# Performance work log

Measured on AMD Instinct MI355X. Metric: run time of the kernel, lower is better.

## Reference

```python
import jax, jax.numpy as jnp
import numpy as np

B = 64          # number of scenes/graphs
OBJS = 2048     # objects per scene
N = B * OBJS    # total objects
D = 256         # representation_dim
K = 2           # num_channels


def setup_inputs() -> dict:
    key = jax.random.key(0)
    k1, k2, k3 = jax.random.split(key, 3)
    x_aggregation = jax.random.normal(k1, (N, D), dtype=jnp.float32)
    num_objs = jnp.full((B,), OBJS, dtype=jnp.int32)
    # glorot for att_shared [1, D]: fan_in + fan_out = 1 + D
    std_shared = float(np.sqrt(6.0 / (1 + D)))
    att_shared = jax.random.uniform(k2, (1, D), dtype=jnp.float32,
                                    minval=-std_shared, maxval=std_shared)
    # glorot for att_scale [K, 1]
    std_scale = float(np.sqrt(6.0 / (K + 1)))
    att_scale = jax.random.uniform(k3, (K, 1), dtype=jnp.float32,
                                   minval=-std_scale, maxval=std_scale)
    channel_bias = jnp.zeros((K, D), dtype=jnp.float32)
    return {"x_aggregation": x_aggregation, "num_objs": num_objs,
            "att_shared": att_shared, "att_scale": att_scale,
            "channel_bias": channel_bias}


def reference(x_aggregation, num_objs, att_shared, att_scale, channel_bias):
    batch_idx = jnp.repeat(jnp.arange(B), num_objs, total_repeat_length=N)  # [N]
    # scatter_mean: per-scene context features [B, D]
    seg_sum = jax.ops.segment_sum(x_aggregation, batch_idx, num_segments=B)
    counts = jnp.maximum(num_objs, 1).astype(x_aggregation.dtype)
    ctx = seg_sum / counts[:, None]
    attn_in = jax.nn.leaky_relu(x_aggregation + ctx[batch_idx], negative_slope=0.2)  # [N, D]
    # per-channel logits: ((attn_in + bias[k]) . att_shared) * scale[k]
    base = attn_in @ att_shared[0]                 # [N]
    bias_term = channel_bias @ att_shared[0]       # [K]
    logits = (base[:, None] + bias_term[None, :]) * att_scale[:, 0][None, :]  # [N, K]
    # per-channel segment softmax over objects within each scene
    m = jax.ops.segment_max(logits, batch_idx, num_segments=B)   # [B, K]
    z = jnp.exp(logits - m[batch_idx])
    s = jax.ops.segment_sum(z, batch_idx, num_segments=B)        # [B, K]
    attn_weights = z / s[batch_idx]                              # [N, K]
    # attention-weighted pooling per channel -> [B, D, K]
    weighted = x_aggregation[:, :, None] * attn_weights[:, None, :]  # [N, D, K]
    scene_features = jax.ops.segment_sum(weighted, batch_idx, num_segments=B)
    return scene_features, attn_weights
```

## Files before the change

kernel.cpp:

```cpp
#include <hip/hip_runtime.h>

#define B    64
#define OBJS 2048
#define NTOT (B * OBJS)
#define D    256
#define K    2
#define S1   16
#define CH   (OBJS / S1)
#define RPW  (CH / 4)

#define WS_P1  0
#define WS_UP  (1024 * 256)
#define WS_ZP  (WS_UP + 1024 * 512)
#define WS_E   (WS_ZP + 1024 * 8)

static __device__ __forceinline__ float lrelu02(float v) {
    return v > 0.0f ? v : 0.2f * v;
}

__global__ __launch_bounds__(256) void k1_partial(const float* __restrict__ x,
                                                  float* __restrict__ ws) {
    __shared__ float red[4 * D];
    int blk = blockIdx.x;
    int w = threadIdx.x >> 6, l = threadIdx.x & 63;
    int row0 = blk * CH + w * RPW;

    float4 acc = make_float4(0.f, 0.f, 0.f, 0.f);
    const float* px = x + (size_t)row0 * D + 4 * l;
#pragma unroll 8
    for (int j = 0; j < RPW; ++j) {
        float4 v = *(const float4*)(px + (size_t)j * D);
        acc.x += v.x; acc.y += v.y; acc.z += v.z; acc.w += v.w;
    }
    *(float4*)(red + w * D + 4 * l) = acc;
    __syncthreads();
    int t = threadIdx.x;
    if (t < 64) {
        float4 a = ((const float4*)(red        ))[t];
        float4 e = ((const float4*)(red +     D))[t];
        float4 f = ((const float4*)(red + 2 * D))[t];
        float4 g = ((const float4*)(red + 3 * D))[t];
        float4 s = make_float4(a.x + e.x + f.x + g.x, a.y + e.y + f.y + g.y,
                               a.z + e.z + f.z + g.z, a.w + e.w + f.w + g.w);
        *(float4*)(ws + WS_P1 + blk * D + 4 * t) = s;
    }
}

__global__ __launch_bounds__(256) void k2_main(const float* __restrict__ x,
                                               const int* __restrict__ num_objs,
                                               const float* __restrict__ att_scale,
                                               const float* __restrict__ att_shared,
                                               const float* __restrict__ channel_bias,
                                               float* __restrict__ ws) {
    __shared__ float pl[4 * 576];
    __shared__ float esm[4 * 16];
    __shared__ float sctx[D];
    __shared__ float sbt[2];

    int blk = blockIdx.x;
    int b = blk >> 4;
    int t = threadIdx.x;
    int w = t >> 6, l = t & 63;
    int r = l & 7, s = l >> 3;
    int row0 = blk * CH + w * RPW;

    {
        int cnt = num_objs[b]; if (cnt < 1) cnt = 1;
        float inv = 1.0f / (float)cnt;
        float sum = 0.f;
#pragma unroll
        for (int c = 0; c < S1; ++c) sum += ws[WS_P1 + (b * S1 + c) * D + t];
        sctx[t] = sum * inv;
    }
    if (t < 64) {
        float4 a = ((const float4*)att_shared)[t];
#pragma unroll
        for (int k = 0; k < K; ++k) {
            float4 cb = ((const float4*)(channel_bias + k * D))[t];
            float v = a.x * cb.x + a.y * cb.y + a.z * cb.z + a.w * cb.w;
#pragma unroll
            for (int m = 32; m > 0; m >>= 1) v += __shfl_xor(v, m);
            if (t == 0) sbt[k] = v;
        }
    }
    __syncthreads();

    float4 a4   = ((const float4*)att_shared)[l];
    float4 ctx4 = *(const float4*)(sctx + 4 * l);
    float bt0 = sbt[0], bt1 = sbt[1];
    float s0 = att_scale[0], s1 = att_scale[1];

    float4 acc0 = make_float4(0.f, 0.f, 0.f, 0.f);
    float4 acc1 = make_float4(0.f, 0.f, 0.f, 0.f);
    float z0 = 0.f, z1 = 0.f;
    float e0c = 0.f, e1c = 0.f;
    float* pw = pl  + w * 576;
    float* ew = esm + w * 16;
    const float* px = x + (size_t)row0 * D + 4 * l;

#pragma unroll
    for (int g = 0; g < 4; ++g) {
        float4 v0 = *(const float4*)(px + (size_t)(g * 8 + 0) * D);
        float4 v1 = *(const float4*)(px + (size_t)(g * 8 + 1) * D);
        float4 v2 = *(const float4*)(px + (size_t)(g * 8 + 2) * D);
        float4 v3 = *(const float4*)(px + (size_t)(g * 8 + 3) * D);
        float4 v4 = *(const float4*)(px + (size_t)(g * 8 + 4) * D);
        float4 v5 = *(const float4*)(px + (size_t)(g * 8 + 5) * D);
        float4 v6 = *(const float4*)(px + (size_t)(g * 8 + 6) * D);
        float4 v7 = *(const float4*)(px + (size_t)(g * 8 + 7) * D);

#define PDOT(V) (lrelu02((V).x + ctx4.x) * a4.x + lrelu02((V).y + ctx4.y) * a4.y \
               + lrelu02((V).z + ctx4.z) * a4.z + lrelu02((V).w + ctx4.w) * a4.w)
        pw[l * 9 + 0] = PDOT(v0); pw[l * 9 + 1] = PDOT(v1);
        pw[l * 9 + 2] = PDOT(v2); pw[l * 9 + 3] = PDOT(v3);
        pw[l * 9 + 4] = PDOT(v4); pw[l * 9 + 5] = PDOT(v5);
        pw[l * 9 + 6] = PDOT(v6); pw[l * 9 + 7] = PDOT(v7);
#undef PDOT
        float tr = 0.f;
#pragma unroll
        for (int q = 0; q < 8; ++q) tr += pw[(s * 8 + q) * 9 + r];
        tr += __shfl_xor(tr, 8);
        tr += __shfl_xor(tr, 16);
        tr += __shfl_xor(tr, 32);

        float e0 = __expf((tr + bt0) * s0);
        float e1 = __expf((tr + bt1) * s1);
        if (((l >> 3) & 3) == g) { e0c = e0; e1c = e1; }
        if (l < 8) { ew[2 * l] = e0; ew[2 * l + 1] = e1; }
        float4 E0 = *(const float4*)(ew + 0);
        float4 E1 = *(const float4*)(ew + 4);
        float4 E2 = *(const float4*)(ew + 8);
        float4 E3 = *(const float4*)(ew + 12);
        z0 += E0.x + E0.z + E1.x + E1.z + E2.x + E2.z + E3.x + E3.z;
        z1 += E0.y + E0.w + E1.y + E1.w + E2.y + E2.w + E3.y + E3.w;

#define ACC(V, EA, EB) { acc0.x += (V).x * (EA); acc0.y += (V).y * (EA);      \
                         acc0.z += (V).z * (EA); acc0.w += (V).w * (EA);      \
                         acc1.x += (V).x * (EB); acc1.y += (V).y * (EB);      \
                         acc1.z += (V).z * (EB); acc1.w += (V).w * (EB); }
        ACC(v0, E0.x, E0.y) ACC(v1, E0.z, E0.w)
        ACC(v2, E1.x, E1.y) ACC(v3, E1.z, E1.w)
        ACC(v4, E2.x, E2.y) ACC(v5, E2.z, E2.w)
        ACC(v6, E3.x, E3.y) ACC(v7, E3.z, E3.w)
#undef ACC
    }

    if (l < 32) ((float2*)(ws + WS_E))[row0 + l] = make_float2(e0c, e1c);
    if (l == 0) {
        ws[WS_ZP + blk * 8 + w * 2 + 0] = z0;
        ws[WS_ZP + blk * 8 + w * 2 + 1] = z1;
    }
    __syncthreads();
    {
        int base = w * (D * K) + l * 8;
        pl[base + 0] = acc0.x; pl[base + 1] = acc1.x;
        pl[base + 2] = acc0.y; pl[base + 3] = acc1.y;
        pl[base + 4] = acc0.z; pl[base + 5] = acc1.z;
        pl[base + 6] = acc0.w; pl[base + 7] = acc1.w;
    }
    __syncthreads();
    if (t < 128) {
        float4 a = ((const float4*)(pl       ))[t];
        float4 e = ((const float4*)(pl +  512))[t];
        float4 f = ((const float4*)(pl + 1024))[t];
        float4 g = ((const float4*)(pl + 1536))[t];
        float4 s4 = make_float4(a.x + e.x + f.x + g.x, a.y + e.y + f.y + g.y,
                                a.z + e.z + f.z + g.z, a.w + e.w + f.w + g.w);
        *(float4*)(ws + WS_UP + (size_t)blk * (D * K) + 4 * t) = s4;
    }
}

__global__ __launch_bounds__(256) void k3_final(const float* __restrict__ ws,
                                                float* __restrict__ out) {
    __shared__ float zsh[2];
    int b = blockIdx.x;
    int t = threadIdx.x;
    int w = t >> 6, l = t & 63;

    if (w < 2) {
        float v = ws[WS_ZP + (b * S1 + (l >> 2)) * 8 + (l & 3) * 2 + w];
#pragma unroll
        for (int m = 32; m > 0; m >>= 1) v += __shfl_xor(v, m);
        if (l == 0) zsh[w] = v;
    }
    __syncthreads();
    float z0 = zsh[0], z1 = zsh[1];
    float iz0 = 1.0f / z0, iz1 = 1.0f / z1;

#pragma unroll
    for (int j = t; j < D * K; j += 256) {
        float s = 0.f;
#pragma unroll
        for (int c = 0; c < S1; ++c) s += ws[WS_UP + (b * S1 + c) * (D * K) + j];
        out[b * (D * K) + j] = s * ((j & 1) ? iz1 : iz0);
    }
    const float4* E = (const float4*)(ws + WS_E);
    float4* W = (float4*)(out + B * D * K);
#pragma unroll
    for (int i = t; i < OBJS / 2; i += 256) {
        float4 e = E[b * (OBJS / 2) + i];
        W[b * (OBJS / 2) + i] = make_float4(e.x * iz0, e.y * iz1, e.z * iz0, e.w * iz1);
    }
}

extern "C" void kernel_launch(void* const* d_in, const int* in_sizes, int n_in,
                              void* d_out, int out_size, void* d_ws, size_t ws_size,
                              hipStream_t stream) {
    const float* x            = (const float*)d_in[0];
    const int*   num_objs     = (const int*)d_in[1];
    const float* att_shared   = (const float*)d_in[2];
    const float* att_scale    = (const float*)d_in[3];
    const float* channel_bias = (const float*)d_in[4];
    float* ws  = (float*)d_ws;
    float* out = (float*)d_out;

    k1_partial<<<B * S1, 256, 0, stream>>>(x, ws);
    k2_main<<<B * S1, 256, 0, stream>>>(x, num_objs, att_scale, att_shared,
                                        channel_bias, ws);
    k3_final<<<B, 256, 0, stream>>>(ws, out);
}
```

Before: 221.4 us.

## Fuse three kernels into one cooperative kernel with per-scene atomic barriers

Merges the partial-sum, main attention, and final normalization kernels into a single cooperative launch. Blocks of one scene sync on an atomic counter spin-wait before computing context, and the last block of each scene to finish (found with a second atomic counter) does the final reduction and write-out. This removes two kernel launch boundaries and their tail idle time. In exchange it adds a memset, spin-wait costs, and a dependence on all 1024 blocks being co-resident.

```diff
diff --git a/kernel.cpp b/kernel.cpp
--- a/kernel.cpp
+++ b/kernel.cpp
@@ -13,9 +13,205 @@
 #define WS_UP  (1024 * 256)
 #define WS_ZP  (WS_UP + 1024 * 512)
 #define WS_E   (WS_ZP + 1024 * 8)
+#define WS_CNT (WS_E + NTOT * 2)
 
 static __device__ __forceinline__ float lrelu02(float v) {
     return v > 0.0f ? v : 0.2f * v;
+}
+
+__global__ __launch_bounds__(256, 4) void fused_all(
+        const float* __restrict__ x,
+        const int* __restrict__ num_objs,
+        const float* __restrict__ att_scale,
+        const float* __restrict__ att_shared,
+        const float* __restrict__ channel_bias,
+        float* __restrict__ ws,
+        float* __restrict__ out) {
+    __shared__ float pl[4 * 576];
+    __shared__ float esm[4 * 16];
+    __shared__ float sctx[D];
+    __shared__ float sbt[2];
+    __shared__ int   sfin;
+
+    int blk = blockIdx.x;
+    int b = blk >> 4;
+    int t = threadIdx.x;
+    int w = t >> 6, l = t & 63;
+    int r = l & 7, sl = l >> 3;
+    int row0 = blk * CH + w * RPW;
+    int* cntA = (int*)(ws + WS_CNT);
+    int* cntF = cntA + B;
+
+    {
+        float4 acc = make_float4(0.f, 0.f, 0.f, 0.f);
+        const float* px = x + (size_t)row0 * D + 4 * l;
+#pragma unroll 8
+        for (int j = 0; j < RPW; ++j) {
+            float4 v = *(const float4*)(px + (size_t)j * D);
+            acc.x += v.x; acc.y += v.y; acc.z += v.z; acc.w += v.w;
+        }
+        *(float4*)(pl + w * D + 4 * l) = acc;
+        __syncthreads();
+        if (t < 64) {
+            float4 a = ((const float4*)(pl        ))[t];
+            float4 e = ((const float4*)(pl +     D))[t];
+            float4 f = ((const float4*)(pl + 2 * D))[t];
+            float4 g = ((const float4*)(pl + 3 * D))[t];
+            float4 s4 = make_float4(a.x + e.x + f.x + g.x, a.y + e.y + f.y + g.y,
+                                    a.z + e.z + f.z + g.z, a.w + e.w + f.w + g.w);
+            *(float4*)(ws + WS_P1 + blk * D + 4 * t) = s4;
+        }
+        __syncthreads();
+        if (t == 0) {
+            __threadfence();
+            atomicAdd(&cntA[b], 1);
+            while (__hip_atomic_load(&cntA[b], __ATOMIC_RELAXED,
+                                     __HIP_MEMORY_SCOPE_AGENT) < S1)
+                __builtin_amdgcn_s_sleep(2);
+            __threadfence();
+        }
+        __syncthreads();
+    }
+
+    {
+        int cnt = num_objs[b]; if (cnt < 1) cnt = 1;
+        float inv = 1.0f / (float)cnt;
+        float sum = 0.f;
+#pragma unroll
+        for (int c = 0; c < S1; ++c) sum += ws[WS_P1 + (b * S1 + c) * D + t];
+        sctx[t] = sum * inv;
+    }
+    if (t < 64) {
+        float4 a = ((const float4*)att_shared)[t];
+#pragma unroll
+        for (int k = 0; k < K; ++k) {
+            float4 cb = ((const float4*)(channel_bias + k * D))[t];
+            float v = a.x * cb.x + a.y * cb.y + a.z * cb.z + a.w * cb.w;
+#pragma unroll
+            for (int m = 32; m > 0; m >>= 1) v += __shfl_xor(v, m);
+            if (t == 0) sbt[k] = v;
+        }
+    }
+    __syncthreads();
+
+    float4 a4   = ((const float4*)att_shared)[l];
+    float4 ctx4 = *(const float4*)(sctx + 4 * l);
+    float bt0 = sbt[0], bt1 = sbt[1];
+    float s0 = att_scale[0], s1 = att_scale[1];
+
+    float4 acc0 = make_float4(0.f, 0.f, 0.f, 0.f);
+    float4 acc1 = make_float4(0.f, 0.f, 0.f, 0.f);
+    float z0 = 0.f, z1 = 0.f;
+    float e0c = 0.f, e1c = 0.f;
+    float* pw = pl  + w * 576;
+    float* ew = esm + w * 16;
+    const float* px = x + (size_t)row0 * D + 4 * l;
+
+#pragma unroll
+    for (int g = 0; g < 4; ++g) {
+        float4 v0 = *(const float4*)(px + (size_t)(g * 8 + 0) * D);
+        float4 v1 = *(const float4*)(px + (size_t)(g * 8 + 1) * D);
+        float4 v2 = *(const float4*)(px + (size_t)(g * 8 + 2) * D);
+        float4 v3 = *(const float4*)(px + (size_t)(g * 8 + 3) * D);
+        float4 v4 = *(const float4*)(px + (size_t)(g * 8 + 4) * D);
+        float4 v5 = *(const float4*)(px + (size_t)(g * 8 + 5) * D);
+        float4 v6 = *(const float4*)(px + (size_t)(g * 8 + 6) * D);
+        float4 v7 = *(const float4*)(px + (size_t)(g * 8 + 7) * D);
+
+#define PDOT(V) (lrelu02((V).x + ctx4.x) * a4.x + lrelu02((V).y + ctx4.y) * a4.y \
+               + lrelu02((V).z + ctx4.z) * a4.z + lrelu02((V).w + ctx4.w) * a4.w)
+        pw[l * 9 + 0] = PDOT(v0); pw[l * 9 + 1] = PDOT(v1);
+        pw[l * 9 + 2] = PDOT(v2); pw[l * 9 + 3] = PDOT(v3);
+        pw[l * 9 + 4] = PDOT(v4); pw[l * 9 + 5] = PDOT(v5);
+        pw[l * 9 + 6] = PDOT(v6); pw[l * 9 + 7] = PDOT(v7);
+#undef PDOT
+        float tr = 0.f;
+#pragma unroll
+        for (int q = 0; q < 8; ++q) tr += pw[(sl * 8 + q) * 9 + r];
+        tr += __shfl_xor(tr, 8);
+        tr += __shfl_xor(tr, 16);
+        tr += __shfl_xor(tr, 32);
+
+        float e0 = __expf((tr + bt0) * s0);
+        float e1 = __expf((tr + bt1) * s1);
+        if (((l >> 3) & 3) == g) { e0c = e0; e1c = e1; }
+        if (l < 8) { ew[2 * l] = e0; ew[2 * l + 1] = e1; }
+        float4 E0 = *(const float4*)(ew + 0);
+        float4 E1 = *(const float4*)(ew + 4);
+        float4 E2 = *(const float4*)(ew + 8);
+        float4 E3 = *(const float4*)(ew + 12);
+        z0 += E0.x + E0.z + E1.x + E1.z + E2.x + E2.z + E3.x + E3.z;
+        z1 += E0.y + E0.w + E1.y + E1.w + E2.y + E2.w + E3.y + E3.w;
+
+#define ACC(V, EA, EB) { acc0.x += (V).x * (EA); acc0.y += (V).y * (EA);      \
+                         acc0.z += (V).z * (EA); acc0.w += (V).w * (EA);      \
+                         acc1.x += (V).x * (EB); acc1.y += (V).y * (EB);      \
+                         acc1.z += (V).z * (EB); acc1.w += (V).w * (EB); }
+        ACC(v0, E0.x, E0.y) ACC(v1, E0.z, E0.w)
+        ACC(v2, E1.x, E1.y) ACC(v3, E1.z, E1.w)
+        ACC(v4, E2.x, E2.y) ACC(v5, E2.z, E2.w)
+        ACC(v6, E3.x, E3.y) ACC(v7, E3.z, E3.w)
+#undef ACC
+    }
+
+    if (l < 32) ((float2*)(ws + WS_E))[row0 + l] = make_float2(e0c, e1c);
+    if (l == 0) {
+        ws[WS_ZP + blk * 8 + w * 2 + 0] = z0;
+        ws[WS_ZP + blk * 8 + w * 2 + 1] = z1;
+    }
+    __syncthreads();
+    {
+        int base = w * (D * K) + l * 8;
+        pl[base + 0] = acc0.x; pl[base + 1] = acc1.x;
+        pl[base + 2] = acc0.y; pl[base + 3] = acc1.y;
+        pl[base + 4] = acc0.z; pl[base + 5] = acc1.z;
+        pl[base + 6] = acc0.w; pl[base + 7] = acc1.w;
+    }
+    __syncthreads();
+    if (t < 128) {
+        float4 a = ((const float4*)(pl       ))[t];
+        float4 e = ((const float4*)(pl +  512))[t];
+        float4 f = ((const float4*)(pl + 1024))[t];
+        float4 g = ((const float4*)(pl + 1536))[t];
+        float4 s4 = make_float4(a.x + e.x + f.x + g.x, a.y + e.y + f.y + g.y,
+                                a.z + e.z + f.z + g.z, a.w + e.w + f.w + g.w);
+        *(float4*)(ws + WS_UP + (size_t)blk * (D * K) + 4 * t) = s4;
+    }
+
+    __syncthreads();
+    if (t == 0) {
+        __threadfence();
+        int old = atomicAdd(&cntF[b], 1);
+        sfin = (old == S1 - 1) ? 1 : 0;
+        if (sfin) __threadfence();
+    }
+    __syncthreads();
+    if (!sfin) return;
+
+    if (w < 2) {
+        float v = ws[WS_ZP + (b * S1 + (l >> 2)) * 8 + (l & 3) * 2 + w];
+#pragma unroll
+        for (int m = 32; m > 0; m >>= 1) v += __shfl_xor(v, m);
+        if (l == 0) sbt[w] = v;
+    }
+    __syncthreads();
+    float zf0 = sbt[0], zf1 = sbt[1];
+    float iz0 = 1.0f / zf0, iz1 = 1.0f / zf1;
+
+#pragma unroll
+    for (int j = t; j < D * K; j += 256) {
+        float ssum = 0.f;
+#pragma unroll
+        for (int c = 0; c < S1; ++c) ssum += ws[WS_UP + (b * S1 + c) * (D * K) + j];
+        out[b * (D * K) + j] = ssum * ((j & 1) ? iz1 : iz0);
+    }
+    const float4* E = (const float4*)(ws + WS_E);
+    float4* W = (float4*)(out + B * D * K);
+#pragma unroll
+    for (int i = t; i < OBJS / 2; i += 256) {
+        float4 e4 = E[b * (OBJS / 2) + i];
+        W[b * (OBJS / 2) + i] = make_float4(e4.x * iz0, e4.y * iz1, e4.z * iz0, e4.w * iz1);
+    }
 }
 
 __global__ __launch_bounds__(256) void k1_partial(const float* __restrict__ x,
@@ -214,6 +410,27 @@
     float* ws  = (float*)d_ws;
     float* out = (float*)d_out;
 
+    static int coop_ok = -1;
+    if (coop_ok < 0) {
+        int nb = 0;
+        hipError_t e = hipOccupancyMaxActiveBlocksPerMultiprocessor(
+                &nb, fused_all, 256, 0);
+        coop_ok = (e == hipSuccess && nb >= 4) ? 1 : 0;
+    }
+
+    if (coop_ok) {
+        hipMemsetAsync((char*)d_ws + sizeof(float) * (size_t)WS_CNT, 0,
+                       2 * B * sizeof(int), stream);
+        void* args[] = {(void*)&x, (void*)&num_objs, (void*)&att_scale,
+                        (void*)&att_shared, (void*)&channel_bias,
+                        (void*)&ws, (void*)&out};
+        hipError_t e = hipLaunchCooperativeKernel((void*)fused_all,
+                                                  dim3(B * S1), dim3(256),
+                                                  args, 0, stream);
+        if (e == hipSuccess) return;
+        coop_ok = 0;
+    }
+
     k1_partial<<<B * S1, 256, 0, stream>>>(x, ws);
     k2_main<<<B * S1, 256, 0, stream>>>(x, num_objs, att_scale, att_shared,
                                         channel_bias, ws);
```

Result: no change. 222.3 us (+0.4%).
